# Performance work log

Measured on AMD Instinct MI355X. Metric: run time of the kernel, lower is better.

The kernel has to match this reference:

```python
import jax, jax.numpy as jnp
from jax import lax
import numpy as np

N_CENTER, N_NEAR, COUT = 1024, 32, 256


def fps(xyz, m):
    # farthest point sampling -> [B, m] int32 indices
    B, N, _ = xyz.shape
    dist0 = jnp.full((B, N), 1e10, xyz.dtype)
    far0 = jnp.zeros((B,), jnp.int32)

    def step(carry, _):
        dists, far = carry
        cen = jax.vmap(lambda p, i: p[i])(xyz, far)            # [B,3]
        d = jnp.sum((xyz - cen[:, None, :]) ** 2, axis=-1)     # [B,N]
        dists = jnp.minimum(dists, d)
        nxt = jnp.argmax(dists, axis=-1).astype(jnp.int32)
        return (dists, nxt), far

    _, idx = lax.scan(step, (dist0, far0), None, length=m)
    return jnp.transpose(idx)                                   # [B,m]


def knn(xyz, k):
    # euclidean kNN over all points -> [B,N,k] (stand-in for surface_knn)
    sq = jnp.sum(xyz ** 2, axis=-1)                             # [B,N]
    d = sq[:, :, None] + sq[:, None, :] - 2.0 * jnp.einsum('bnd,bmd->bnm', xyz, xyz)
    _, idx = lax.top_k(-d, k)
    return idx


def gather(x, idx):
    # index_points: x [B,N,...], idx [B,S] or [B,S,K]
    return jax.vmap(lambda p, i: p[i])(x, idx)


def point_attention(center_fea, group_fea, wq, wk, wv):
    # center_fea [B,S,Cin], group_fea [B,S,K,D] -> [B,S,COUT]
    q = jnp.einsum('bsc,ch->bsh', center_fea, wq)
    k = jnp.einsum('bskd,dh->bskh', group_fea, wk)
    v = jnp.einsum('bskd,dh->bskh', group_fea, wv)
    scores = jnp.einsum('bsh,bskh->bsk', q, k) / jnp.sqrt(jnp.asarray(COUT, q.dtype))
    attn = jax.nn.softmax(scores, axis=-1)
    return jnp.einsum('bsk,bskh->bsh', attn, v)


def _forward(xyz, mad, adj, pt, mad_fea, adj_fea, pt_fea, cst_fea,
             wq_mad, wk_mad, wv_mad, wq_adj, wk_adj, wv_adj,
             wq_pt, wk_pt, wv_pt, wq_cst, wk_cst, wv_cst):
    idx_all = knn(xyz, N_NEAR)                  # [B,N,K]
    fps_idx = fps(xyz, N_CENTER)                # [B,S]

    center_xyz = gather(xyz, fps_idx)
    center_mad = gather(mad, fps_idx)
    center_adj = gather(adj, fps_idx)
    center_pt = gather(pt, fps_idx)
    c_mad_fea = gather(mad_fea, fps_idx)
    c_adj_fea = gather(adj_fea, fps_idx)
    c_pt_fea = gather(pt_fea, fps_idx)
    c_cst_fea = gather(cst_fea, fps_idx)

    idx = gather(idx_all, fps_idx)              # [B,S,K]
    g_xyz = gather(xyz, idx)
    g_mad = gather(mad, idx)
    g_adj = gather(adj, idx)
    g_pt = gather(pt, idx)
    g_mad_fea = gather(mad_fea, idx)
    g_adj_fea = gather(adj_fea, idx)
    g_pt_fea = gather(pt_fea, idx)
    g_cst_fea = gather(cst_fea, idx)

    mad_rel = g_mad - center_mad[:, :, None, :]
    adj_cat = jnp.concatenate([g_adj, jnp.broadcast_to(center_adj[:, :, None, :], g_adj.shape)], axis=-1)
    pt_cat = jnp.concatenate([g_pt, jnp.broadcast_to(center_pt[:, :, None, :], g_pt.shape)], axis=-1)
    xyz_rel = g_xyz - center_xyz[:, :, None, :]

    g_mad_fea = jnp.concatenate([g_mad_fea, mad_rel], axis=-1)
    g_adj_fea = jnp.concatenate([g_adj_fea, adj_cat], axis=-1)
    g_pt_fea = jnp.concatenate([g_pt_fea, pt_cat], axis=-1)
    g_cst_fea = jnp.concatenate([g_cst_fea, xyz_rel], axis=-1)

    o_mad = point_attention(c_mad_fea, g_mad_fea, wq_mad, wk_mad, wv_mad)
    o_adj = point_attention(c_adj_fea, g_adj_fea, wq_adj, wk_adj, wv_adj)
    o_pt = point_attention(c_pt_fea, g_pt_fea, wq_pt, wk_pt, wv_pt)
    o_cst = point_attention(c_cst_fea, g_cst_fea, wq_cst, wk_cst, wv_cst)

    return (center_xyz, center_mad, center_adj, center_pt, o_mad, o_adj, o_pt, o_cst)


def setup_inputs() -> dict:
    key = jax.random.key(0)
    ks = jax.random.split(key, 24)
    B, N, C = 4, 4096, 128
    inp = {
        'xyz': jax.random.normal(ks[0], (B, N, 3), jnp.float32),
        'mad': jax.random.normal(ks[1], (B, N, 3), jnp.float32),
        'adj': jax.random.uniform(ks[2], (B, N, 2), jnp.float32),
        'pt': jax.random.uniform(ks[3], (B, N, 4), jnp.float32),
        'mad_fea': jax.random.normal(ks[4], (B, N, C), jnp.float32),
        'adj_fea': jax.random.normal(ks[5], (B, N, C), jnp.float32),
        'pt_fea': jax.random.normal(ks[6], (B, N, C), jnp.float32),
        'cst_fea': jax.random.normal(ks[7], (B, N, C), jnp.float32),
    }
    dims = {'wq_mad': C, 'wk_mad': C + 3, 'wv_mad': C + 3,
            'wq_adj': C, 'wk_adj': C + 4, 'wv_adj': C + 4,
            'wq_pt': C, 'wk_pt': C + 8, 'wv_pt': C + 8,
            'wq_cst': C, 'wk_cst': C + 3, 'wv_cst': C + 3}
    for i, (name, d) in enumerate(dims.items()):
        inp[name] = jax.random.normal(ks[8 + i], (d, COUT), jnp.float32) * 0.02
    return inp


def reference(xyz, mad, adj, pt, mad_fea, adj_fea, pt_fea, cst_fea,
              wq_mad, wk_mad, wv_mad, wq_adj, wk_adj, wv_adj,
              wq_pt, wk_pt, wv_pt, wq_cst, wk_cst, wv_cst):
    return _forward(xyz, mad, adj, pt, mad_fea, adj_fea, pt_fea, cst_fea,
                    wq_mad, wk_mad, wv_mad, wq_adj, wk_adj, wv_adj,
                    wq_pt, wk_pt, wv_pt, wq_cst, wk_cst, wv_cst)
```

## Files before the change

kernel.cpp:

```cpp
#include <hip/hip_runtime.h>

#define BATCH 4
#define NPTS  4096
#define NC    1024
#define KNN   32
#define CIN   128
#define CO    256
#define DP    136

#define OFF_CXYZ 0
#define OFF_CMAD (BATCH*NC*3)
#define OFF_CADJ (OFF_CMAD + BATCH*NC*3)
#define OFF_CPT  (OFF_CADJ + BATCH*NC*2)
#define OFF_OMAD (OFF_CPT  + BATCH*NC*4)
#define OFF_OADJ (OFF_OMAD + BATCH*NC*CO)
#define OFF_OPT  (OFF_OADJ + BATCH*NC*CO)
#define OFF_OCST (OFF_OPT  + BATCH*NC*CO)

typedef unsigned long long u64;

template<bool MAXI>
__device__ __forceinline__ u64 wave_red_u64(u64 k)
{
    const int oldv = MAXI ? 0 : -1;
#define DPP_STEP(C)                                                              \
    {                                                                            \
        unsigned plo = (unsigned)__builtin_amdgcn_update_dpp(oldv, (int)(unsigned)k,        C, 0xf, 0xf, false); \
        unsigned phi = (unsigned)__builtin_amdgcn_update_dpp(oldv, (int)(unsigned)(k>>32),  C, 0xf, 0xf, false); \
        u64 p = ((u64)phi << 32) | plo;                                          \
        if (MAXI ? (p > k) : (p < k)) k = p;                                     \
    }
    DPP_STEP(0x111) DPP_STEP(0x112) DPP_STEP(0x114)
    DPP_STEP(0x118) DPP_STEP(0x142) DPP_STEP(0x143)
#undef DPP_STEP
    return k;
}

__global__ __launch_bounds__(256) void fps_prep_kernel(
    const float* __restrict__ xyz, int* __restrict__ fps_idx,
    const float* __restrict__ wq_mad, const float* __restrict__ wk_mad, const float* __restrict__ wv_mad,
    const float* __restrict__ wq_adj, const float* __restrict__ wk_adj, const float* __restrict__ wv_adj,
    const float* __restrict__ wq_pt,  const float* __restrict__ wk_pt,  const float* __restrict__ wv_pt,
    const float* __restrict__ wq_cst, const float* __restrict__ wk_cst, const float* __restrict__ wv_cst,
    float* __restrict__ M, float* __restrict__ Wvp)
{
    __shared__ float4 s_xyz[NPTS];
    __shared__ u64    s_ck[2][4];
    const int t = threadIdx.x;

    if (blockIdx.x >= BATCH) {
        const int r    = blockIdx.x - BATCH;
        const int type = r / DP;
        const int row  = r - type * DP;
        const float* wq; const float* wk; const float* wv; int D;
        if (type == 0)      { wq=wq_mad; wk=wk_mad; wv=wv_mad; D=131; }
        else if (type == 1) { wq=wq_adj; wk=wk_adj; wv=wv_adj; D=132; }
        else if (type == 2) { wq=wq_pt;  wk=wk_pt;  wv=wv_pt;  D=136; }
        else                { wq=wq_cst; wk=wk_cst; wv=wv_cst; D=131; }

        Wvp[((size_t)type*DP + row)*CO + t] = (row < D) ? wv[(size_t)row*CO + t] : 0.f;

        if (row < CIN) {
            float* sq = (float*)s_xyz;
            sq[t] = wq[(size_t)row*CO + t];
            __syncthreads();
            if (t < DP) {
                float acc = 0.f;
                if (t < D) {
                    const float* wkr = wk + (size_t)t * CO;
                    for (int h = 0; h < CO; h += 4) {
                        float4 a = *(const float4*)&wkr[h];
                        float4 b4 = *(const float4*)&sq[h];
                        acc = fmaf(a.x,b4.x,acc); acc = fmaf(a.y,b4.y,acc);
                        acc = fmaf(a.z,b4.z,acc); acc = fmaf(a.w,b4.w,acc);
                    }
                }
                M[((size_t)type*CIN + row)*DP + t] = acc;
            }
        }
        return;
    }

    const int b = blockIdx.x;
    const float* xb = xyz + (size_t)b * NPTS * 3;

    float px[16], py[16], pz[16], dd[16];
    unsigned inv[16];
#pragma unroll
    for (int i = 0; i < 16; ++i) {
        int p = t + i * 256;
        px[i] = xb[p*3+0]; py[i] = xb[p*3+1]; pz[i] = xb[p*3+2];
        s_xyz[p] = make_float4(px[i], py[i], pz[i], 0.f);
        dd[i] = 1e10f;
        inv[i] = ~(unsigned)p;
    }
    __syncthreads();

    int far = 0;
    float cx = xb[0], cy = xb[1], cz = xb[2];
    for (int s = 0; s < NC; ++s) {
        if (t == 0) fps_idx[b*NC + s] = far;
        u64 K[16];
#pragma unroll
        for (int i = 0; i < 16; ++i) {
            float dx = __fsub_rn(px[i], cx);
            float dy = __fsub_rn(py[i], cy);
            float dz = __fsub_rn(pz[i], cz);
            float d  = __fadd_rn(__fadd_rn(__fmul_rn(dx,dx), __fmul_rn(dy,dy)), __fmul_rn(dz,dz));
            float nd = fminf(dd[i], d);
            dd[i] = nd;
            K[i] = ((u64)__float_as_uint(nd) << 32) | inv[i];
        }
#pragma unroll
        for (int st = 8; st >= 1; st >>= 1)
#pragma unroll
            for (int j = 0; j < st; ++j)
                if (K[j+st] > K[j]) K[j] = K[j+st];
        u64 k = wave_red_u64<true>(K[0]);

        const int buf = s & 1;
        if ((t & 63) == 63) s_ck[buf][t>>6] = k;
        __syncthreads();
        u64 k0 = s_ck[buf][0], k1 = s_ck[buf][1], k2 = s_ck[buf][2], k3 = s_ck[buf][3];
        if (k1 > k0) k0 = k1;
        if (k3 > k2) k2 = k3;
        if (k2 > k0) k0 = k2;
        far = (int)~((unsigned)k0);
        float4 c = s_xyz[far];
        cx = c.x; cy = c.y; cz = c.z;
    }
}

__global__ __launch_bounds__(256) void knn_kernel(const float* __restrict__ xyz,
                                                  const int* __restrict__ fps_idx,
                                                  int* __restrict__ nbr_idx)
{
    const int bs = blockIdx.x;
    const int b  = bs >> 10;
    const int t  = threadIdx.x;
    const float* xb = xyz + (size_t)b * NPTS * 3;
    const int ci = fps_idx[bs];
    const float cx = xb[ci*3], cy = xb[ci*3+1], cz = xb[ci*3+2];
    const float sqc = __fadd_rn(__fadd_rn(__fmul_rn(cx,cx), __fmul_rn(cy,cy)), __fmul_rn(cz,cz));

    u64 key[16];
#pragma unroll
    for (int i = 0; i < 16; ++i) {
        int p = t + i * 256;
        float x = xb[p*3], y = xb[p*3+1], z = xb[p*3+2];
        float sqm = __fadd_rn(__fadd_rn(__fmul_rn(x,x), __fmul_rn(y,y)), __fmul_rn(z,z));
        float dot = __fadd_rn(__fadd_rn(__fmul_rn(cx,x), __fmul_rn(cy,y)), __fmul_rn(cz,z));
        float dv  = __fsub_rn(__fadd_rn(sqc, sqm), __fmul_rn(2.0f, dot));
        unsigned u = __float_as_uint(dv);
        u ^= (unsigned)(((int)u >> 31)) | 0x80000000u;
        key[i] = ((u64)u << 32) | (unsigned)p;
    }
    u64 kmin = key[0];
#pragma unroll
    for (int i = 1; i < 16; ++i) if (key[i] < kmin) kmin = key[i];

    __shared__ u64 s_ck[2][4];

    for (int kk = 0; kk < KNN; ++kk) {
        u64 k = wave_red_u64<false>(kmin);
        const int buf = kk & 1;
        if ((t & 63) == 63) s_ck[buf][t>>6] = k;
        __syncthreads();
        u64 k0 = s_ck[buf][0], k1 = s_ck[buf][1], k2 = s_ck[buf][2], k3 = s_ck[buf][3];
        if (k1 < k0) k0 = k1;
        if (k3 < k2) k2 = k3;
        if (k2 < k0) k0 = k2;
        unsigned w = (unsigned)k0;
        if (t == 0) nbr_idx[bs*KNN + kk] = (int)w;
        if ((w & 255u) == (unsigned)t) {
#pragma unroll
            for (int i = 0; i < 16; ++i)
                if (w == (unsigned)(t + i*256)) key[i] = ~0ull;
            u64 m = key[0];
#pragma unroll
            for (int i = 1; i < 16; ++i) if (key[i] < m) m = key[i];
            kmin = m;
        }
    }
}

template<int TYPE>
__device__ __forceinline__ void attn_t(
    int b, int bs0, int ci,
    const float* __restrict__ fea, const float* __restrict__ aux,
    const float* __restrict__ Mt, const float* __restrict__ Wvpt,
    float* __restrict__ outp,
    float (*s_cf)[CIN], float (*s_u)[DP], float (*s_fea)[KNN][DP],
    float (*s_sc)[KNN], float (*s_wf)[DP], const int (*s_nbr4)[KNN])
{
    const int t = threadIdx.x, g = t >> 6, l = t & 63;
    const int l31 = l & 31, h32 = l >> 5;

    if (l < 32) {
        float4 v = *(const float4*)&fea[((size_t)(b*NPTS + ci))*CIN + l*4];
        *(float4*)&s_cf[g][l*4] = v;
    }
#pragma unroll
    for (int it = 0; it < 16; ++it) {
        int kk = it*2 + h32;
        int j  = s_nbr4[g][kk];
        float4 v = *(const float4*)&fea[((size_t)(b*NPTS + j))*CIN + l31*4];
        *(float4*)&s_fea[g][kk][l31*4] = v;
    }
    if (l < KNN) {
        int j = s_nbr4[g][l];
        float pad[8];
        if (TYPE == 0 || TYPE == 3) {
#pragma unroll
            for (int i = 0; i < 3; ++i)
                pad[i] = aux[(size_t)(b*NPTS + j)*3 + i] - aux[(size_t)(b*NPTS + ci)*3 + i];
            pad[3]=pad[4]=pad[5]=pad[6]=pad[7]=0.f;
        } else if (TYPE == 1) {
            pad[0] = aux[(size_t)(b*NPTS + j)*2 + 0];
            pad[1] = aux[(size_t)(b*NPTS + j)*2 + 1];
            pad[2] = aux[(size_t)(b*NPTS + ci)*2 + 0];
            pad[3] = aux[(size_t)(b*NPTS + ci)*2 + 1];
            pad[4]=pad[5]=pad[6]=pad[7]=0.f;
        } else {
#pragma unroll
            for (int i = 0; i < 4; ++i) pad[i]   = aux[(size_t)(b*NPTS + j)*4 + i];
#pragma unroll
            for (int i = 0; i < 4; ++i) pad[4+i] = aux[(size_t)(b*NPTS + ci)*4 + i];
        }
#pragma unroll
        for (int i = 0; i < 8; ++i) s_fea[g][l][CIN+i] = pad[i];
    }
    __syncthreads();

#pragma unroll
    for (int j = 0; j < 3; ++j) {
        int d = l + 64*j;
        if (d < DP) {
            float acc = 0.f;
            for (int c = 0; c < CIN; c += 4) {
                float4 cf4 = *(const float4*)&s_cf[g][c];
                acc = fmaf(cf4.x, Mt[(size_t)(c+0)*DP + d], acc);
                acc = fmaf(cf4.y, Mt[(size_t)(c+1)*DP + d], acc);
                acc = fmaf(cf4.z, Mt[(size_t)(c+2)*DP + d], acc);
                acc = fmaf(cf4.w, Mt[(size_t)(c+3)*DP + d], acc);
            }
            s_u[g][d] = acc;
        }
    }
    __syncthreads();

#pragma unroll
    for (int it = 0; it < 16; ++it) {
        int kk = it*2 + h32;
        float acc = 0.f;
        for (int c = l31; c < DP/4; c += 32) {
            float4 f4 = *(const float4*)&s_fea[g][kk][c*4];
            float4 u4 = *(const float4*)&s_u[g][c*4];
            acc = fmaf(f4.x,u4.x,acc); acc = fmaf(f4.y,u4.y,acc);
            acc = fmaf(f4.z,u4.z,acc); acc = fmaf(f4.w,u4.w,acc);
        }
#pragma unroll
        for (int off = 16; off; off >>= 1) acc += __shfl_xor(acc, off);
        if (l31 == 0) s_sc[g][kk] = acc * 0.0625f;
    }
    __syncthreads();

    if (l < KNN) {
        float sc = s_sc[g][l];
        float m = sc;
#pragma unroll
        for (int off = 16; off; off >>= 1) m = fmaxf(m, __shfl_xor(m, off));
        float e = expf(sc - m);
        float ssum = e;
#pragma unroll
        for (int off = 16; off; off >>= 1) ssum += __shfl_xor(ssum, off);
        s_sc[g][l] = e / ssum;
    }
    __syncthreads();

    if (l < DP/4) {
        const int d0 = l*4;
        float w0=0.f, w1=0.f, w2=0.f, w3=0.f;
#pragma unroll
        for (int k4 = 0; k4 < KNN; k4 += 4) {
            float4 a  = *(const float4*)&s_sc[g][k4];
            float4 f0 = *(const float4*)&s_fea[g][k4+0][d0];
            float4 f1 = *(const float4*)&s_fea[g][k4+1][d0];
            float4 f2 = *(const float4*)&s_fea[g][k4+2][d0];
            float4 f3 = *(const float4*)&s_fea[g][k4+3][d0];
            w0=fmaf(a.x,f0.x,w0); w1=fmaf(a.x,f0.y,w1); w2=fmaf(a.x,f0.z,w2); w3=fmaf(a.x,f0.w,w3);
            w0=fmaf(a.y,f1.x,w0); w1=fmaf(a.y,f1.y,w1); w2=fmaf(a.y,f1.z,w2); w3=fmaf(a.y,f1.w,w3);
            w0=fmaf(a.z,f2.x,w0); w1=fmaf(a.z,f2.y,w1); w2=fmaf(a.z,f2.z,w2); w3=fmaf(a.z,f2.w,w3);
            w0=fmaf(a.w,f3.x,w0); w1=fmaf(a.w,f3.y,w1); w2=fmaf(a.w,f3.z,w2); w3=fmaf(a.w,f3.w,w3);
        }
        s_wf[g][d0+0]=w0; s_wf[g][d0+1]=w1; s_wf[g][d0+2]=w2; s_wf[g][d0+3]=w3;
    }
    __syncthreads();

    float o0=0.f, o1=0.f, o2=0.f, o3=0.f;
    for (int d4 = 0; d4 < DP/4; ++d4) {
        float4 wf0 = *(const float4*)&s_wf[0][d4*4];
        float4 wf1 = *(const float4*)&s_wf[1][d4*4];
        float4 wf2 = *(const float4*)&s_wf[2][d4*4];
        float4 wf3 = *(const float4*)&s_wf[3][d4*4];
        float v0 = Wvpt[(size_t)(d4*4+0)*CO + t];
        float v1 = Wvpt[(size_t)(d4*4+1)*CO + t];
        float v2 = Wvpt[(size_t)(d4*4+2)*CO + t];
        float v3 = Wvpt[(size_t)(d4*4+3)*CO + t];
        o0=fmaf(wf0.x,v0,o0); o0=fmaf(wf0.y,v1,o0); o0=fmaf(wf0.z,v2,o0); o0=fmaf(wf0.w,v3,o0);
        o1=fmaf(wf1.x,v0,o1); o1=fmaf(wf1.y,v1,o1); o1=fmaf(wf1.z,v2,o1); o1=fmaf(wf1.w,v3,o1);
        o2=fmaf(wf2.x,v0,o2); o2=fmaf(wf2.y,v1,o2); o2=fmaf(wf2.z,v2,o2); o2=fmaf(wf2.w,v3,o2);
        o3=fmaf(wf3.x,v0,o3); o3=fmaf(wf3.y,v1,o3); o3=fmaf(wf3.z,v2,o3); o3=fmaf(wf3.w,v3,o3);
    }
    outp[(size_t)(bs0+0)*CO + t] = o0;
    outp[(size_t)(bs0+1)*CO + t] = o1;
    outp[(size_t)(bs0+2)*CO + t] = o2;
    outp[(size_t)(bs0+3)*CO + t] = o3;
    __syncthreads();
}

__global__ __launch_bounds__(256) void attn_kernel(
    const float* __restrict__ xyz, const float* __restrict__ mad,
    const float* __restrict__ adj, const float* __restrict__ pt,
    const float* __restrict__ mad_fea, const float* __restrict__ adj_fea,
    const float* __restrict__ pt_fea,  const float* __restrict__ cst_fea,
    const float* __restrict__ M, const float* __restrict__ Wvp,
    const int* __restrict__ fps_idx, const int* __restrict__ nbr_idx,
    float* __restrict__ out)
{
    __shared__ float s_cf[4][CIN];
    __shared__ float s_u[4][DP];
    __shared__ float s_fea[4][KNN][DP];
    __shared__ float s_sc[4][KNN];
    __shared__ float s_wf[4][DP];
    __shared__ int   s_nbr4[4][KNN];
    __shared__ int   s_ci4[4];

    const int bs0 = blockIdx.x * 4;
    const int b   = bs0 >> 10;
    const int t   = threadIdx.x;
    const int g   = t >> 6, l = t & 63;

    if (t < 4) s_ci4[t] = fps_idx[bs0 + t];
    if (t < 128) s_nbr4[t>>5][t&31] = nbr_idx[(bs0 + (t>>5))*KNN + (t&31)];
    __syncthreads();
    const int ci = s_ci4[g];

    if (l < 3)             out[OFF_CXYZ + (bs0+g)*3 + l]      = xyz[(size_t)(b*NPTS+ci)*3 + l];
    if (l >= 4 && l < 7)   out[OFF_CMAD + (bs0+g)*3 + (l-4)]  = mad[(size_t)(b*NPTS+ci)*3 + (l-4)];
    if (l >= 8 && l < 10)  out[OFF_CADJ + (bs0+g)*2 + (l-8)]  = adj[(size_t)(b*NPTS+ci)*2 + (l-8)];
    if (l >= 12 && l < 16) out[OFF_CPT  + (bs0+g)*4 + (l-12)] = pt[(size_t)(b*NPTS+ci)*4 + (l-12)];

    attn_t<0>(b, bs0, ci, mad_fea, mad, M + 0*CIN*DP, Wvp + 0*DP*CO, out + OFF_OMAD,
              s_cf, s_u, s_fea, s_sc, s_wf, s_nbr4);
    attn_t<1>(b, bs0, ci, adj_fea, adj, M + 1*CIN*DP, Wvp + 1*DP*CO, out + OFF_OADJ,
              s_cf, s_u, s_fea, s_sc, s_wf, s_nbr4);
    attn_t<2>(b, bs0, ci, pt_fea,  pt,  M + 2*CIN*DP, Wvp + 2*DP*CO, out + OFF_OPT,
              s_cf, s_u, s_fea, s_sc, s_wf, s_nbr4);
    attn_t<3>(b, bs0, ci, cst_fea, xyz, M + 3*CIN*DP, Wvp + 3*DP*CO, out + OFF_OCST,
              s_cf, s_u, s_fea, s_sc, s_wf, s_nbr4);
}

extern "C" void kernel_launch(void* const* d_in, const int* in_sizes, int n_in,
                              void* d_out, int out_size, void* d_ws, size_t ws_size,
                              hipStream_t stream)
{
    const float* xyz     = (const float*)d_in[0];
    const float* mad     = (const float*)d_in[1];
    const float* adj     = (const float*)d_in[2];
    const float* pt      = (const float*)d_in[3];
    const float* mad_fea = (const float*)d_in[4];
    const float* adj_fea = (const float*)d_in[5];
    const float* pt_fea  = (const float*)d_in[6];
    const float* cst_fea = (const float*)d_in[7];
    const float* wq_mad  = (const float*)d_in[8];
    const float* wk_mad  = (const float*)d_in[9];
    const float* wv_mad  = (const float*)d_in[10];
    const float* wq_adj  = (const float*)d_in[11];
    const float* wk_adj  = (const float*)d_in[12];
    const float* wv_adj  = (const float*)d_in[13];
    const float* wq_pt   = (const float*)d_in[14];
    const float* wk_pt   = (const float*)d_in[15];
    const float* wv_pt   = (const float*)d_in[16];
    const float* wq_cst  = (const float*)d_in[17];
    const float* wk_cst  = (const float*)d_in[18];
    const float* wv_cst  = (const float*)d_in[19];
    float* out = (float*)d_out;

    int*   fps_idx = (int*)d_ws;
    int*   nbr_idx = fps_idx + BATCH*NC;
    float* M       = (float*)(nbr_idx + BATCH*NC*KNN);
    float* Wvp     = M + 4*CIN*DP;

    fps_prep_kernel<<<BATCH + 4*DP, 256, 0, stream>>>(xyz, fps_idx,
        wq_mad, wk_mad, wv_mad, wq_adj, wk_adj, wv_adj,
        wq_pt, wk_pt, wv_pt, wq_cst, wk_cst, wv_cst, M, Wvp);
    knn_kernel<<<BATCH*NC, 256, 0, stream>>>(xyz, fps_idx, nbr_idx);
    attn_kernel<<<BATCH*NC/4, 256, 0, stream>>>(xyz, mad, adj, pt,
        mad_fea, adj_fea, pt_fea, cst_fea, M, Wvp, fps_idx, nbr_idx, out);
}
```

Baseline: 1.121 ms.

## Fuse FPS, kNN and attention into a persistent ticketed megakernel with dataflow flags

Merges the FPS, kNN and attention kernels into one launch. Blocks take an atomic ticket to pick a role, and consumers spin on per-center flags, so kNN for a sampled center and attention for a finished group can start while FPS is still producing later centers. This targets the serialized long FPS phase, which leaves most of the GPU idle. In exchange it adds two memsets, spin-wait polling, and a 86KB shared allocation for every block, which lowers occupancy for the kNN and attention roles.

```diff
diff --git a/kernel.cpp b/kernel.cpp
--- a/kernel.cpp
+++ b/kernel.cpp
@@ -36,52 +36,51 @@
     return k;
 }
 
-__global__ __launch_bounds__(256) void fps_prep_kernel(
-    const float* __restrict__ xyz, int* __restrict__ fps_idx,
+__global__ __launch_bounds__(256) void prep_kernel(
     const float* __restrict__ wq_mad, const float* __restrict__ wk_mad, const float* __restrict__ wv_mad,
     const float* __restrict__ wq_adj, const float* __restrict__ wk_adj, const float* __restrict__ wv_adj,
     const float* __restrict__ wq_pt,  const float* __restrict__ wk_pt,  const float* __restrict__ wv_pt,
     const float* __restrict__ wq_cst, const float* __restrict__ wk_cst, const float* __restrict__ wv_cst,
     float* __restrict__ M, float* __restrict__ Wvp)
 {
-    __shared__ float4 s_xyz[NPTS];
-    __shared__ u64    s_ck[2][4];
+    __shared__ float sq[CO];
     const int t = threadIdx.x;
-
-    if (blockIdx.x >= BATCH) {
-        const int r    = blockIdx.x - BATCH;
-        const int type = r / DP;
-        const int row  = r - type * DP;
-        const float* wq; const float* wk; const float* wv; int D;
-        if (type == 0)      { wq=wq_mad; wk=wk_mad; wv=wv_mad; D=131; }
-        else if (type == 1) { wq=wq_adj; wk=wk_adj; wv=wv_adj; D=132; }
-        else if (type == 2) { wq=wq_pt;  wk=wk_pt;  wv=wv_pt;  D=136; }
-        else                { wq=wq_cst; wk=wk_cst; wv=wv_cst; D=131; }
-
-        Wvp[((size_t)type*DP + row)*CO + t] = (row < D) ? wv[(size_t)row*CO + t] : 0.f;
-
-        if (row < CIN) {
-            float* sq = (float*)s_xyz;
-            sq[t] = wq[(size_t)row*CO + t];
-            __syncthreads();
-            if (t < DP) {
-                float acc = 0.f;
-                if (t < D) {
-                    const float* wkr = wk + (size_t)t * CO;
-                    for (int h = 0; h < CO; h += 4) {
-                        float4 a = *(const float4*)&wkr[h];
-                        float4 b4 = *(const float4*)&sq[h];
-                        acc = fmaf(a.x,b4.x,acc); acc = fmaf(a.y,b4.y,acc);
-                        acc = fmaf(a.z,b4.z,acc); acc = fmaf(a.w,b4.w,acc);
-                    }
+    const int r    = blockIdx.x;
+    const int type = r / DP;
+    const int row  = r - type * DP;
+    const float* wq; const float* wk; const float* wv; int D;
+    if (type == 0)      { wq=wq_mad; wk=wk_mad; wv=wv_mad; D=131; }
+    else if (type == 1) { wq=wq_adj; wk=wk_adj; wv=wv_adj; D=132; }
+    else if (type == 2) { wq=wq_pt;  wk=wk_pt;  wv=wv_pt;  D=136; }
+    else                { wq=wq_cst; wk=wk_cst; wv=wv_cst; D=131; }
+
+    Wvp[((size_t)type*DP + row)*CO + t] = (row < D) ? wv[(size_t)row*CO + t] : 0.f;
+
+    if (row < CIN) {
+        sq[t] = wq[(size_t)row*CO + t];
+        __syncthreads();
+        if (t < DP) {
+            float acc = 0.f;
+            if (t < D) {
+                const float* wkr = wk + (size_t)t * CO;
+                for (int h = 0; h < CO; h += 4) {
+                    float4 a = *(const float4*)&wkr[h];
+                    float4 b4 = *(const float4*)&sq[h];
+                    acc = fmaf(a.x,b4.x,acc); acc = fmaf(a.y,b4.y,acc);
+                    acc = fmaf(a.z,b4.z,acc); acc = fmaf(a.w,b4.w,acc);
                 }
-                M[((size_t)type*CIN + row)*DP + t] = acc;
             }
-        }
-        return;
-    }
-
-    const int b = blockIdx.x;
+            M[((size_t)type*CIN + row)*DP + t] = acc;
+        }
+    }
+}
+
+__device__ __forceinline__ void fps_role(int b, const float* __restrict__ xyz,
+                                         int* __restrict__ fps_idx, char* s_raw)
+{
+    float4* s_xyz   = (float4*)s_raw;
+    u64 (*s_ck)[4]  = (u64(*)[4])(s_raw + NPTS*16);
+    const int t = threadIdx.x;
     const float* xb = xyz + (size_t)b * NPTS * 3;
 
     float px[16], py[16], pz[16], dd[16];
@@ -99,7 +98,8 @@
     int far = 0;
     float cx = xb[0], cy = xb[1], cz = xb[2];
     for (int s = 0; s < NC; ++s) {
-        if (t == 0) fps_idx[b*NC + s] = far;
+        if (t == 0)
+            __hip_atomic_store(&fps_idx[(b<<10) + s], far, __ATOMIC_RELAXED, __HIP_MEMORY_SCOPE_AGENT);
         u64 K[16];
 #pragma unroll
         for (int i = 0; i < 16; ++i) {
@@ -131,15 +131,29 @@
     }
 }
 
-__global__ __launch_bounds__(256) void knn_kernel(const float* __restrict__ xyz,
-                                                  const int* __restrict__ fps_idx,
-                                                  int* __restrict__ nbr_idx)
-{
-    const int bs = blockIdx.x;
-    const int b  = bs >> 10;
+__device__ __forceinline__ void knn_role(int n, const float* __restrict__ xyz,
+                                         int* __restrict__ fps_idx,
+                                         int* __restrict__ nbr_idx,
+                                         int* __restrict__ knn_done, char* s_raw)
+{
+    u64 (*s_ck)[4] = (u64(*)[4])s_raw;
+    int* s_ci      = (int*)(s_raw + 64);
+
+    const int b  = n & 3;
+    const int s  = n >> 2;
+    const int bs = (b << 10) + s;
     const int t  = threadIdx.x;
+
+    if (t == 0) {
+        int v;
+        while ((v = __hip_atomic_load(&fps_idx[bs], __ATOMIC_RELAXED, __HIP_MEMORY_SCOPE_AGENT)) < 0)
+            __builtin_amdgcn_s_sleep(2);
+        *s_ci = v;
+    }
+    __syncthreads();
+    const int ci = *s_ci;
+
     const float* xb = xyz + (size_t)b * NPTS * 3;
-    const int ci = fps_idx[bs];
     const float cx = xb[ci*3], cy = xb[ci*3+1], cz = xb[ci*3+2];
     const float sqc = __fadd_rn(__fadd_rn(__fmul_rn(cx,cx), __fmul_rn(cy,cy)), __fmul_rn(cz,cz));
 
@@ -158,8 +172,6 @@
     u64 kmin = key[0];
 #pragma unroll
     for (int i = 1; i < 16; ++i) if (key[i] < kmin) kmin = key[i];
-
-    __shared__ u64 s_ck[2][4];
 
     for (int kk = 0; kk < KNN; ++kk) {
         u64 k = wave_red_u64<false>(kmin);
@@ -171,7 +183,8 @@
         if (k3 < k2) k2 = k3;
         if (k2 < k0) k0 = k2;
         unsigned w = (unsigned)k0;
-        if (t == 0) nbr_idx[bs*KNN + kk] = (int)w;
+        if (t == 0)
+            __hip_atomic_store(&nbr_idx[bs*KNN + kk], (int)w, __ATOMIC_RELAXED, __HIP_MEMORY_SCOPE_AGENT);
         if ((w & 255u) == (unsigned)t) {
 #pragma unroll
             for (int i = 0; i < 16; ++i)
@@ -182,6 +195,8 @@
             kmin = m;
         }
     }
+    if (t == 0)
+        __hip_atomic_store(&knn_done[bs], 1, __ATOMIC_RELEASE, __HIP_MEMORY_SCOPE_AGENT);
 }
 
 template<int TYPE>
@@ -319,30 +334,37 @@
     __syncthreads();
 }
 
-__global__ __launch_bounds__(256) void attn_kernel(
+__device__ __forceinline__ void attn_role(int a,
     const float* __restrict__ xyz, const float* __restrict__ mad,
     const float* __restrict__ adj, const float* __restrict__ pt,
     const float* __restrict__ mad_fea, const float* __restrict__ adj_fea,
     const float* __restrict__ pt_fea,  const float* __restrict__ cst_fea,
     const float* __restrict__ M, const float* __restrict__ Wvp,
-    const int* __restrict__ fps_idx, const int* __restrict__ nbr_idx,
-    float* __restrict__ out)
-{
-    __shared__ float s_cf[4][CIN];
-    __shared__ float s_u[4][DP];
-    __shared__ float s_fea[4][KNN][DP];
-    __shared__ float s_sc[4][KNN];
-    __shared__ float s_wf[4][DP];
-    __shared__ int   s_nbr4[4][KNN];
-    __shared__ int   s_ci4[4];
-
-    const int bs0 = blockIdx.x * 4;
-    const int b   = bs0 >> 10;
+    int* __restrict__ fps_idx, int* __restrict__ nbr_idx, int* __restrict__ knn_done,
+    float* __restrict__ out, char* s_raw)
+{
+    float (*s_cf)[CIN]      = (float(*)[CIN])     (s_raw);
+    float (*s_u)[DP]        = (float(*)[DP])      (s_raw + 2048);
+    float (*s_fea)[KNN][DP] = (float(*)[KNN][DP]) (s_raw + 4224);
+    float (*s_sc)[KNN]      = (float(*)[KNN])     (s_raw + 73856);
+    float (*s_wf)[DP]       = (float(*)[DP])      (s_raw + 74368);
+    int   (*s_nbr4)[KNN]    = (int(*)[KNN])       (s_raw + 76544);
+    int   *s_ci4            = (int*)              (s_raw + 77056);
+
+    const int b   = a & 3;
+    const int bs0 = (b << 10) + ((a >> 2) << 2);
     const int t   = threadIdx.x;
     const int g   = t >> 6, l = t & 63;
 
-    if (t < 4) s_ci4[t] = fps_idx[bs0 + t];
-    if (t < 128) s_nbr4[t>>5][t&31] = nbr_idx[(bs0 + (t>>5))*KNN + (t&31)];
+    if (t < 4) {
+        while (__hip_atomic_load(&knn_done[bs0 + t], __ATOMIC_ACQUIRE, __HIP_MEMORY_SCOPE_AGENT) == 0)
+            __builtin_amdgcn_s_sleep(2);
+        s_ci4[t] = __hip_atomic_load(&fps_idx[bs0 + t], __ATOMIC_RELAXED, __HIP_MEMORY_SCOPE_AGENT);
+    }
+    __syncthreads();
+    if (t < 128)
+        s_nbr4[t>>5][t&31] =
+            __hip_atomic_load(&nbr_idx[(bs0 + (t>>5))*KNN + (t&31)], __ATOMIC_RELAXED, __HIP_MEMORY_SCOPE_AGENT);
     __syncthreads();
     const int ci = s_ci4[g];
 
@@ -359,6 +381,37 @@
               s_cf, s_u, s_fea, s_sc, s_wf, s_nbr4);
     attn_t<3>(b, bs0, ci, cst_fea, xyz, M + 3*CIN*DP, Wvp + 3*DP*CO, out + OFF_OCST,
               s_cf, s_u, s_fea, s_sc, s_wf, s_nbr4);
+}
+
+__global__ __launch_bounds__(256) void mega_kernel(
+    const float* __restrict__ xyz, const float* __restrict__ mad,
+    const float* __restrict__ adj, const float* __restrict__ pt,
+    const float* __restrict__ mad_fea, const float* __restrict__ adj_fea,
+    const float* __restrict__ pt_fea,  const float* __restrict__ cst_fea,
+    const float* __restrict__ M, const float* __restrict__ Wvp,
+    int* __restrict__ fps_idx, int* __restrict__ nbr_idx,
+    int* __restrict__ knn_done, int* __restrict__ ticket,
+    float* __restrict__ out)
+{
+    __shared__ __align__(16) char s_raw[86016];
+    __shared__ int s_ticket;
+    const int t = threadIdx.x;
+    if (t == 0) s_ticket = atomicAdd(ticket, 1);
+    __syncthreads();
+    const int T = s_ticket;
+
+    if (T < BATCH) {
+        fps_role(T, xyz, fps_idx, s_raw);
+        return;
+    }
+    const int u = T - BATCH;
+    const int q = u / 5;
+    const int r = u - q * 5;
+    if (r < 4)
+        knn_role(q*4 + r, xyz, fps_idx, nbr_idx, knn_done, s_raw);
+    else
+        attn_role(q, xyz, mad, adj, pt, mad_fea, adj_fea, pt_fea, cst_fea,
+                  M, Wvp, fps_idx, nbr_idx, knn_done, out, s_raw);
 }
 
 extern "C" void kernel_launch(void* const* d_in, const int* in_sizes, int n_in,
@@ -387,15 +440,21 @@
     const float* wv_cst  = (const float*)d_in[19];
     float* out = (float*)d_out;
 
-    int*   fps_idx = (int*)d_ws;
-    int*   nbr_idx = fps_idx + BATCH*NC;
-    float* M       = (float*)(nbr_idx + BATCH*NC*KNN);
-    float* Wvp     = M + 4*CIN*DP;
-
-    fps_prep_kernel<<<BATCH + 4*DP, 256, 0, stream>>>(xyz, fps_idx,
+    int*   fps_idx  = (int*)d_ws;
+    int*   knn_done = fps_idx + BATCH*NC;
+    int*   ticket   = knn_done + BATCH*NC;
+    int*   nbr_idx  = ticket + 64;
+    float* M        = (float*)(nbr_idx + BATCH*NC*KNN);
+    float* Wvp      = M + 4*CIN*DP;
+
+    hipMemsetAsync(fps_idx, 0xFF, (size_t)BATCH*NC*sizeof(int), stream);
+    hipMemsetAsync(knn_done, 0, (size_t)(BATCH*NC + 64)*sizeof(int), stream);
+
+    prep_kernel<<<4*DP, 256, 0, stream>>>(
         wq_mad, wk_mad, wv_mad, wq_adj, wk_adj, wv_adj,
         wq_pt, wk_pt, wv_pt, wq_cst, wk_cst, wv_cst, M, Wvp);
-    knn_kernel<<<BATCH*NC, 256, 0, stream>>>(xyz, fps_idx, nbr_idx);
-    attn_kernel<<<BATCH*NC/4, 256, 0, stream>>>(xyz, mad, adj, pt,
-        mad_fea, adj_fea, pt_fea, cst_fea, M, Wvp, fps_idx, nbr_idx, out);
-}
+
+    mega_kernel<<<BATCH + 5*(BATCH*NC/4), 256, 0, stream>>>(
+        xyz, mad, adj, pt, mad_fea, adj_fea, pt_fea, cst_fea,
+        M, Wvp, fps_idx, nbr_idx, knn_done, ticket, out);
+}
```

Measured after the change: 1.411 ms. +25.8%, slower.
